# Performance work log

Hardware: AMD Instinct MI355X
Metric: run time of the kernel (lower is better)

The kernel has to match this reference:

```python
import jax, jax.numpy as jnp
import numpy as np

S, B, D, H = 2048, 32, 256, 4
EPS = 1e-5


def setup_inputs() -> dict:
    key = jax.random.key(0)
    ks = jax.random.split(key, 16)
    f32 = jnp.float32

    def w(k, shape, scale=0.05):
        return jax.random.normal(k, shape, dtype=f32) * scale

    return {
        "q": jax.random.normal(ks[0], (S, B, D), f32),
        "k": jax.random.normal(ks[1], (S, B, D), f32),
        "v": jax.random.normal(ks[2], (S, B, D), f32),
        # per-head q/k/v projections, stacked over heads [H, D, D]
        "wq": w(ks[3], (H, D, D)), "bq": jnp.zeros((H, D), f32),
        "wk": w(ks[4], (H, D, D)), "bk": jnp.zeros((H, D), f32),
        "wv": w(ks[5], (H, D, D)), "bv": jnp.zeros((H, D), f32),
        # linear_w[i] = BN -> ReLU -> Linear -> BN -> ReLU -> Linear
        "g1": jnp.ones((H, D), f32), "be1": jnp.zeros((H, D), f32),
        "wl1": w(ks[6], (H, D, D)), "bl1": jnp.zeros((H, D), f32),
        "g2": jnp.ones((H, D), f32), "be2": jnp.zeros((H, D), f32),
        "wl2": w(ks[7], (H, D, D)), "bl2": jnp.zeros((H, D), f32),
        # final MLP: [D*H -> D -> D -> D]
        "mw0": w(ks[8], (D, D * H)), "mb0": jnp.zeros((D,), f32),
        "mw1": w(ks[9], (D, D)), "mb1": jnp.zeros((D,), f32),
        "mw2": w(ks[10], (D, D)), "mb2": jnp.zeros((D,), f32),
    }


def _bn(x, gamma, beta):
    # BatchNorm1d in training mode on permuted [B, D, S] tensor == per-channel
    # normalization over (S, B) axes of the [S, B, D] tensor; biased variance.
    m = x.mean(axis=(0, 1))
    v = x.var(axis=(0, 1))
    return (x - m) * jax.lax.rsqrt(v + EPS) * gamma + beta


def _lin(x, W, b):
    return x @ W.T + b


def reference(q, k, v, wq, bq, wk, bk, wv, bv, g1, be1, wl1, bl1,
              g2, be2, wl2, bl2, mw0, mb0, mw1, mb1, mw2, mb2):
    H_ = wq.shape[0]
    xs = []
    for i in range(H_):
        # NOTE: original code reassigns q/k/v, so projections chain across heads
        q = _lin(q, wq[i], bq[i])
        k = _lin(k, wk[i], bk[i])
        v = _lin(v, wv[i], bv[i])
        w = k - q                                  # [S, B, D]
        w = jax.nn.relu(_bn(w, g1[i], be1[i]))
        w = _lin(w, wl1[i], bl1[i])
        w = jax.nn.relu(_bn(w, g2[i], be2[i]))
        w = _lin(w, wl2[i], bl2[i])
        w = jax.nn.softmax(w, axis=0)              # softmax over seq dim
        xs.append((w * v).sum(axis=0))             # [B, D]
    x = jnp.concatenate(xs, axis=-1)[None]         # [1, B, H*D]
    x = jax.nn.relu(_lin(x, mw0, mb0))
    x = jax.nn.relu(_lin(x, mw1, mb1))
    x = _lin(x, mw2, mb2)                          # [1, B, D]
    return x
```

## Files before the change

kernel.cpp:

```cpp
#include <hip/hip_runtime.h>
#include <hip/hip_bf16.h>


typedef short  s16x8 __attribute__((ext_vector_type(8)));
typedef float  f32x4 __attribute__((ext_vector_type(4)));
typedef unsigned short u16;

constexpr int NC = 16;

__device__ __forceinline__ float bu2f(u16 u) {
    union { unsigned int i; float f; } c; c.i = ((unsigned int)u) << 16; return c.f;
}
__device__ __forceinline__ float bs2f(short s) { return bu2f((u16)s); }
__device__ __forceinline__ u16 f2bu(float f) {
    union { float f; unsigned int i; } c; c.f = f;
    unsigned int u = c.i;
    u += 0x7fffu + ((u >> 16) & 1u);
    return (u16)(u >> 16);
}
__device__ __forceinline__ unsigned int pack2(float a, float b) {
    __hip_bfloat162 h = __float22bfloat162_rn(make_float2(a, b));
    union { __hip_bfloat162 h; unsigned int u; } c; c.h = h; return c.u;
}

__global__ __launch_bounds__(256) void detect_k(const unsigned int* __restrict__ qw,
                                                int* __restrict__ flag)
{
    __shared__ int cnt[256];
    const int t = threadIdx.x;
    int c = 0;
    for (int i = 0; i < 64; i++) {
        const unsigned int w = qw[t + i * 256];
        const unsigned int e = (w >> 7) & 0xFFu;
        c += (e >= 96u && e <= 141u) ? 1 : 0;
    }
    cnt[t] = c;
    __syncthreads();
    for (int s = 128; s > 0; s >>= 1) {
        if (t < s) cnt[t] += cnt[t + s];
        __syncthreads();
    }
    if (t == 0) *flag = (cnt[0] > 8192) ? 1 : 0;
}

__global__ __launch_bounds__(256) void wconv_k(
    const void* w0, const void* w1, const void* w2, const void* w3, const void* w4,
    const int* __restrict__ dflag, u16* __restrict__ dst)
{
    const void* srcs[5] = {w0, w1, w2, w3, w4};
    const int y = blockIdx.y;
    const int idx = blockIdx.x * 1024 + threadIdx.x * 4;
    u16* d = dst + y * 262144 + idx;
    if (*dflag == 0) {
        f32x4 v = *(const f32x4*)((const float*)srcs[y] + idx);
        unsigned int lo = pack2(v[0], v[1]);
        unsigned int hi = pack2(v[2], v[3]);
        *(unsigned long long*)d = ((unsigned long long)hi << 32) | lo;
    } else {
        *(unsigned long long*)d = *(const unsigned long long*)((const u16*)srcs[y] + idx);
    }
}

template<int AM, bool EXTA, int STATS>
__device__ __forceinline__ void gemm_core(
    const u16* __restrict__ A, const float* __restrict__ Af,
    const u16* __restrict__ A2, const u16* __restrict__ Qd,
    const u16* __restrict__ Wb,
    const u16* __restrict__ bias16, const float* __restrict__ biasf,
    const u16* __restrict__ g16, const float* __restrict__ gf,
    const u16* __restrict__ be16, const float* __restrict__ bef,
    const float* __restrict__ statsIn, float* __restrict__ statsOut,
    const int f32in, u16* __restrict__ C, const int bx)
{
    __shared__ __align__(16) u16 smem[8192];
    __shared__ float sc_s[256], sh_s[256];
    __shared__ float red_s[256];
    u16* As = smem;
    u16* Bs = smem + 2048;

    const int tid   = threadIdx.x;
    const int tileN = bx & 1;
    const int tileM = bx >> 1;
    const int lane  = tid & 63;
    const int wave  = tid >> 6;
    const int wm    = wave & 1;
    const int wn    = wave >> 1;
    const int lrow  = lane & 15;
    const int quad  = lane >> 4;

    if constexpr (AM != 0) {
        const int c = tid;
        float s = 0.f, q = 0.f;
#pragma unroll
        for (int i = 0; i < NC; i++) {
            s += statsIn[i * 256 + c];
            q += statsIn[(NC + i) * 256 + c];
        }
        const float mean = s * (1.f / 65536.f);
        const float var  = q * (1.f / 65536.f) - mean * mean;
        const float rstd = rsqrtf(var + 1e-5f);
        const float gg = f32in ? gf[c] : bu2f(g16[c]);
        const float bb = f32in ? bef[c] : bu2f(be16[c]);
        sc_s[c] = rstd * gg;
        sh_s[c] = bb - mean * rstd * gg;
        __syncthreads();
    }

    f32x4 acc[2][4];
#pragma unroll
    for (int i = 0; i < 2; i++)
#pragma unroll
        for (int j = 0; j < 4; j++) acc[i][j] = (f32x4){0.f, 0.f, 0.f, 0.f};

    const int  rA   = tid >> 2;
    const int  kq   = (tid & 3) << 3;
    const long rowA = (long)tileM * 64;
    const int  rowB = tileN * 128;

    for (int k0 = 0; k0 < 256; k0 += 32) {
        if (k0) __syncthreads();
        {
            const u16* gw = Wb + (rowB + rA) * 256 + k0 + kq;
            __builtin_amdgcn_global_load_lds(
                (const __attribute__((address_space(1))) void*)gw,
                (__attribute__((address_space(3))) void*)(Bs + tid * 8), 16, 0, 0);
            __builtin_amdgcn_global_load_lds(
                (const __attribute__((address_space(1))) void*)(gw + 64 * 256),
                (__attribute__((address_space(3))) void*)(Bs + 2048 + tid * 8), 16, 0, 0);
        }
        const long offA = (rowA + rA) * 256 + k0 + kq;
        if constexpr (AM == 0) {
            if (EXTA && f32in) {
                const float* p = Af + offA;
                f32x4 a = *(const f32x4*)p;
                f32x4 b = *(const f32x4*)(p + 4);
                union { s16x8 v; unsigned int w[4]; } o;
                o.w[0] = pack2(a[0], a[1]); o.w[1] = pack2(a[2], a[3]);
                o.w[2] = pack2(b[0], b[1]); o.w[3] = pack2(b[2], b[3]);
                *(s16x8*)(As + tid * 8) = o.v;
            } else {
                __builtin_amdgcn_global_load_lds(
                    (const __attribute__((address_space(1))) void*)(A + offA),
                    (__attribute__((address_space(3))) void*)(As + tid * 8), 16, 0, 0);
            }
        } else {
            s16x8 xv = *(const s16x8*)(A + offA);
            s16x8 yv;
            if constexpr (AM == 1) yv = *(const s16x8*)(A2 + offA);
            float d[8];
#pragma unroll
            for (int e = 0; e < 8; e++) {
                float x = bs2f(xv[e]);
                if constexpr (AM == 1) x -= bs2f(yv[e]);
                d[e] = fmaxf(fmaf(x, sc_s[k0 + kq + e], sh_s[k0 + kq + e]), 0.f);
            }
            union { s16x8 v; unsigned int w[4]; } o;
            o.w[0] = pack2(d[0], d[1]); o.w[1] = pack2(d[2], d[3]);
            o.w[2] = pack2(d[4], d[5]); o.w[3] = pack2(d[6], d[7]);
            *(s16x8*)(As + tid * 8) = o.v;
        }
        __syncthreads();

        s16x8 af[2], bf[4];
#pragma unroll
        for (int im = 0; im < 2; im++)
            af[im] = *(const s16x8*)(As + (wm * 32 + im * 16 + lrow) * 32 + quad * 8);
#pragma unroll
        for (int in = 0; in < 4; in++)
            bf[in] = *(const s16x8*)(Bs + (wn * 64 + in * 16 + lrow) * 32 + quad * 8);
#pragma unroll
        for (int im = 0; im < 2; im++)
#pragma unroll
            for (int in = 0; in < 4; in++)
                acc[im][in] = __builtin_amdgcn_mfma_f32_16x16x32_bf16(
                    af[im], bf[in], acc[im][in], 0, 0, 0);
    }

    __syncthreads();
    u16* Cs = smem;
#pragma unroll
    for (int in = 0; in < 4; in++) {
        const int col  = wn * 64 + in * 16 + lrow;
        const int gcol = rowB + col;
        const float bv = f32in ? biasf[gcol] : bu2f(bias16[gcol]);
#pragma unroll
        for (int im = 0; im < 2; im++) {
            const int r0 = wm * 32 + im * 16 + quad * 4;
#pragma unroll
            for (int e = 0; e < 4; e++)
                Cs[(r0 + e) * 128 + col] = f2bu(acc[im][in][e] + bv);
        }
    }
    __syncthreads();

    if constexpr (STATS != 0) {
        const int colL = tid & 127;
        const int half = tid >> 7;
        float s = 0.f, qs = 0.f;
#pragma unroll 4
        for (int r = half * 32; r < half * 32 + 32; r++) {
            float x = bu2f(Cs[r * 128 + colL]);
            if constexpr (STATS == 1) x -= bu2f(Qd[(rowA + r) * 256 + rowB + colL]);
            s += x; qs += x * x;
        }
        red_s[tid] = s;
        __syncthreads();
        float sTot = 0.f;
        if (tid < 128) sTot = red_s[tid] + red_s[tid + 128];
        __syncthreads();
        red_s[tid] = qs;
        __syncthreads();
        if (tid < 128) {
            const float qTot = red_s[tid] + red_s[tid + 128];
            const int copy = tileM & (NC - 1);
            atomicAdd(&statsOut[copy * 256 + rowB + colL], sTot);
            atomicAdd(&statsOut[(NC + copy) * 256 + rowB + colL], qTot);
        }
    }

#pragma unroll
    for (int it = 0; it < 4; it++) {
        const int r  = it * 16 + (tid >> 4);
        const int c8 = (tid & 15) * 8;
        *(s16x8*)(C + (rowA + r) * 256 + rowB + c8) = *(const s16x8*)(Cs + r * 128 + c8);
    }
}

template<int AM, bool EXTA, int STATS>
__global__ __launch_bounds__(256) void gemm_k(
    const u16* A, const float* Af, const u16* A2, const u16* Qd,
    const u16* Wb, const void* bias, const void* g, const void* be, int hoff,
    const float* statsIn, float* statsOut, const int* dflag, u16* C)
{
    const int f32in = (*dflag == 0);
    gemm_core<AM, EXTA, STATS>(A, Af, A2, Qd, Wb,
        (const u16*)bias + hoff, (const float*)bias + hoff,
        (const u16*)g + hoff,    (const float*)g + hoff,
        (const u16*)be + hoff,   (const float*)be + hoff,
        statsIn, statsOut, f32in, C, blockIdx.x);
}

template<bool EXTA>
__global__ __launch_bounds__(256) void proj2_k(
    const u16* A0, const float* A0f, const u16* W0, const void* b0, u16* C0,
    const u16* A1, const float* A1f, const u16* W1, const void* b1, u16* C1,
    int hoff, const int* dflag)
{
    const int f32in = (*dflag == 0);
    const int y = blockIdx.y;
    gemm_core<0, EXTA, 0>(
        y ? A1 : A0, y ? A1f : A0f, nullptr, nullptr, y ? W1 : W0,
        (const u16*)(y ? b1 : b0) + hoff, (const float*)(y ? b1 : b0) + hoff,
        nullptr, nullptr, nullptr, nullptr, nullptr, nullptr,
        f32in, y ? C1 : C0, blockIdx.x);
}

__global__ __launch_bounds__(256) void softmax_chunk_k(
    const u16* __restrict__ L, const u16* __restrict__ V,
    float* __restrict__ pm, float* __restrict__ pl, float* __restrict__ pa)
{
    const int d = threadIdx.x, b = blockIdx.x, ch = blockIdx.y;
    float m = -3.0e38f, l = 0.f, acc = 0.f;
    const long base = ((long)ch * 64 * 32 + b) * 256 + d;
    for (int si = 0; si < 64; si++) {
        const long idx = base + (long)si * 32 * 256;
        const float x = bu2f(L[idx]);
        const float v = bu2f(V[idx]);
        const float mn = fmaxf(m, x);
        const float c  = __expf(m - mn);
        const float e  = __expf(x - mn);
        l   = l * c + e;
        acc = acc * c + e * v;
        m = mn;
    }
    const int p = (ch * 32 + b) * 256 + d;
    pm[p] = m; pl[p] = l; pa[p] = acc;
}

__global__ __launch_bounds__(256) void softmax_merge_k(
    const float* __restrict__ pm, const float* __restrict__ pl,
    const float* __restrict__ pa, float* __restrict__ xcat, int head)
{
    const int d = threadIdx.x, b = blockIdx.x;
    float M = -3.0e38f, L = 0.f, A = 0.f;
    for (int ch = 0; ch < 32; ch++) {
        const int p = (ch * 32 + b) * 256 + d;
        const float m = pm[p], l = pl[p], a = pa[p];
        const float mn = fmaxf(M, m);
        const float c1 = __expf(M - mn), c2 = __expf(m - mn);
        L = L * c1 + l * c2;
        A = A * c1 + a * c2;
        M = mn;
    }
    xcat[b * 1024 + head * 256 + d] = A / L;
}

__global__ __launch_bounds__(256) void mlp_k(
    const float* __restrict__ xcat,
    const u16* __restrict__ mw0, const float* __restrict__ mw0f,
    const u16* __restrict__ mb0, const float* __restrict__ mb0f,
    const u16* __restrict__ mw1, const float* __restrict__ mw1f,
    const u16* __restrict__ mb1, const float* __restrict__ mb1f,
    const u16* __restrict__ mw2, const float* __restrict__ mw2f,
    const u16* __restrict__ mb2, const float* __restrict__ mb2f,
    const int* __restrict__ dflag,
    u16* __restrict__ out, float* __restrict__ outf)
{
    __shared__ float h0[1024];
    __shared__ float h1[256];
    __shared__ float h2[256];
    const int f32in = (*dflag == 0);
    const int j = threadIdx.x, b = blockIdx.x;
#pragma unroll
    for (int i = 0; i < 4; i++) h0[j + i * 256] = xcat[b * 1024 + j + i * 256];
    __syncthreads();

    float a0 = f32in ? mb0f[j] : bu2f(mb0[j]);
    if (f32in) {
        for (int k4 = 0; k4 < 256; k4++) {
            f32x4 wv = *(const f32x4*)(mw0f + j * 1024 + k4 * 4);
#pragma unroll
            for (int e = 0; e < 4; e++) a0 += h0[k4 * 4 + e] * wv[e];
        }
    } else {
        for (int k8 = 0; k8 < 128; k8++) {
            s16x8 wv = *(const s16x8*)(mw0 + j * 1024 + k8 * 8);
#pragma unroll
            for (int e = 0; e < 8; e++) a0 += h0[k8 * 8 + e] * bs2f(wv[e]);
        }
    }
    h1[j] = fmaxf(a0, 0.f);
    __syncthreads();

    float a1 = f32in ? mb1f[j] : bu2f(mb1[j]);
    if (f32in) {
        for (int k4 = 0; k4 < 64; k4++) {
            f32x4 wv = *(const f32x4*)(mw1f + j * 256 + k4 * 4);
#pragma unroll
            for (int e = 0; e < 4; e++) a1 += h1[k4 * 4 + e] * wv[e];
        }
    } else {
        for (int k8 = 0; k8 < 32; k8++) {
            s16x8 wv = *(const s16x8*)(mw1 + j * 256 + k8 * 8);
#pragma unroll
            for (int e = 0; e < 8; e++) a1 += h1[k8 * 8 + e] * bs2f(wv[e]);
        }
    }
    h2[j] = fmaxf(a1, 0.f);
    __syncthreads();

    float a2 = f32in ? mb2f[j] : bu2f(mb2[j]);
    if (f32in) {
        for (int k4 = 0; k4 < 64; k4++) {
            f32x4 wv = *(const f32x4*)(mw2f + j * 256 + k4 * 4);
#pragma unroll
            for (int e = 0; e < 4; e++) a2 += h2[k4 * 4 + e] * wv[e];
        }
    } else {
        for (int k8 = 0; k8 < 32; k8++) {
            s16x8 wv = *(const s16x8*)(mw2 + j * 256 + k8 * 8);
#pragma unroll
            for (int e = 0; e < 8; e++) a2 += h2[k8 * 8 + e] * bs2f(wv[e]);
        }
    }
    if (f32in) outf[b * 256 + j] = a2;
    else       out[b * 256 + j] = f2bu(a2);
}

extern "C" void kernel_launch(void* const* d_in, const int* in_sizes, int n_in,
                              void* d_out, int out_size, void* d_ws, size_t ws_size,
                              hipStream_t stream)
{
    const u16 *q16 = (const u16*)d_in[0], *k16 = (const u16*)d_in[1], *v16 = (const u16*)d_in[2];
    const float *qf = (const float*)d_in[0], *kf = (const float*)d_in[1], *vf = (const float*)d_in[2];

    const size_t TEN = 33554432ull;
    const size_t WBF_OFF = 2097152ull;
    const size_t BUF_OFF = 5242880ull;
    if (ws_size < BUF_OFF + 5 * TEN) return;

    char* ws = (char*)d_ws;
    int*   dflag = (int*)ws;
    float* fb    = (float*)ws;
    float* sums  = fb + 256;
    float* xcat  = sums + 8 * 2 * NC * 256;
    u16*   wbf   = (u16*)(ws + WBF_OFF);
    u16* buf[5];
    for (int i = 0; i < 5; i++) buf[i] = (u16*)(ws + BUF_OFF + (size_t)i * TEN);

    const int qsrc[4] = {-1, 0, 3, 1}, qdst[4] = {0, 3, 1, 4};
    const int ksrc[4] = {-1, 1, 4, 2}, kdst[4] = {1, 4, 2, 0};
    const int vsrc[4] = {-1, 2, 0, 3}, vdst[4] = {2, 0, 3, 1};
    const int x1i[4]  = {3, 1, 4, 2},  lgi[4]  = {4, 2, 0, 3};

    detect_k<<<dim3(1), dim3(256), 0, stream>>>((const unsigned int*)d_in[0], dflag);
    hipMemsetAsync(sums, 0, 8 * 2 * NC * 256 * sizeof(float), stream);
    wconv_k<<<dim3(256, 5), dim3(256), 0, stream>>>(
        d_in[3], d_in[5], d_in[7], d_in[11], d_in[15], dflag, wbf);

    for (int h = 0; h < 4; h++) {
        const u16* qi = h ? (const u16*)buf[qsrc[h]] : q16;
        const u16* ki = h ? (const u16*)buf[ksrc[h]] : k16;
        const u16* vi = h ? (const u16*)buf[vsrc[h]] : v16;
        u16* qo = buf[qdst[h]];
        u16* ko = buf[kdst[h]];
        u16* vo = buf[vdst[h]];
        u16* x1b = buf[x1i[h]];
        u16* lgb = buf[lgi[h]];
        const u16* Wq  = wbf + (0 * 4 + h) * 65536;
        const u16* Wk  = wbf + (1 * 4 + h) * 65536;
        const u16* Wv  = wbf + (2 * 4 + h) * 65536;
        const u16* Wl1 = wbf + (3 * 4 + h) * 65536;
        const u16* Wl2 = wbf + (4 * 4 + h) * 65536;
        float* st1 = sums + (h * 2 + 0) * 2 * NC * 256;
        float* st2 = sums + (h * 2 + 1) * 2 * NC * 256;
        float* parts = (float*)x1b;
        const int hoff = h * 256;

        if (h == 0)
            proj2_k<true><<<dim3(2048, 2), dim3(256), 0, stream>>>(
                q16, qf, Wq, d_in[4], qo, v16, vf, Wv, d_in[8], vo, hoff, dflag);
        else
            proj2_k<false><<<dim3(2048, 2), dim3(256), 0, stream>>>(
                qi, nullptr, Wq, d_in[4], qo, vi, nullptr, Wv, d_in[8], vo, hoff, dflag);

        if (h == 0)
            gemm_k<0, true, 1><<<dim3(2048), dim3(256), 0, stream>>>(
                k16, kf, nullptr, qo, Wk, d_in[6], d_in[6], d_in[6], hoff,
                nullptr, st1, dflag, ko);
        else
            gemm_k<0, false, 1><<<dim3(2048), dim3(256), 0, stream>>>(
                ki, nullptr, nullptr, qo, Wk, d_in[6], d_in[6], d_in[6], hoff,
                nullptr, st1, dflag, ko);

        gemm_k<1, false, 2><<<dim3(2048), dim3(256), 0, stream>>>(
            ko, nullptr, qo, nullptr, Wl1, d_in[12], d_in[9], d_in[10], hoff,
            st1, st2, dflag, x1b);

        gemm_k<2, false, 0><<<dim3(2048), dim3(256), 0, stream>>>(
            x1b, nullptr, nullptr, nullptr, Wl2, d_in[16], d_in[13], d_in[14], hoff,
            st2, nullptr, dflag, lgb);

        softmax_chunk_k<<<dim3(32, 32), dim3(256), 0, stream>>>(
            lgb, vo, parts, parts + 262144, parts + 524288);
        softmax_merge_k<<<dim3(32), dim3(256), 0, stream>>>(
            parts, parts + 262144, parts + 524288, xcat, h);
    }
    mlp_k<<<dim3(32), dim3(256), 0, stream>>>(
        xcat,
        (const u16*)d_in[17], (const float*)d_in[17],
        (const u16*)d_in[18], (const float*)d_in[18],
        (const u16*)d_in[19], (const float*)d_in[19],
        (const u16*)d_in[20], (const float*)d_in[20],
        (const u16*)d_in[21], (const float*)d_in[21],
        (const u16*)d_in[22], (const float*)d_in[22],
        dflag, (u16*)d_out, (float*)d_out);
}
```

Baseline: 899.1 us.

## Double-buffer GEMM K-loop tiles in LDS and remap block-to-tile order

Splits the K-loop into stage/compute lambdas with two LDS buffers, so the next 32-wide K slice is loaded while MFMAs run on the current one. This removes one barrier per iteration and overlaps global-load latency with compute. It also remaps the block index so consecutive blocks are spread across tile rows, likely for XCD/cache locality. LDS use grows to 24KB, which may reduce occupancy.

```diff
diff --git a/kernel.cpp b/kernel.cpp
--- a/kernel.cpp
+++ b/kernel.cpp
@@ -72,15 +72,14 @@
     const float* __restrict__ statsIn, float* __restrict__ statsOut,
     const int f32in, u16* __restrict__ C, const int bx)
 {
-    __shared__ __align__(16) u16 smem[8192];
+    __shared__ __align__(16) u16 smem[12288];
     __shared__ float sc_s[256], sh_s[256];
     __shared__ float red_s[256];
-    u16* As = smem;
-    u16* Bs = smem + 2048;
 
     const int tid   = threadIdx.x;
-    const int tileN = bx & 1;
-    const int tileM = bx >> 1;
+    const int work  = ((bx & 7) << 8) | (bx >> 3);
+    const int tileN = work & 1;
+    const int tileM = work >> 1;
     const int lane  = tid & 63;
     const int wave  = tid >> 6;
     const int wm    = wave & 1;
@@ -117,26 +116,25 @@
     const long rowA = (long)tileM * 64;
     const int  rowB = tileN * 128;
 
-    for (int k0 = 0; k0 < 256; k0 += 32) {
-        if (k0) __syncthreads();
-        {
-            const u16* gw = Wb + (rowB + rA) * 256 + k0 + kq;
-            __builtin_amdgcn_global_load_lds(
-                (const __attribute__((address_space(1))) void*)gw,
-                (__attribute__((address_space(3))) void*)(Bs + tid * 8), 16, 0, 0);
-            __builtin_amdgcn_global_load_lds(
-                (const __attribute__((address_space(1))) void*)(gw + 64 * 256),
-                (__attribute__((address_space(3))) void*)(Bs + 2048 + tid * 8), 16, 0, 0);
-        }
+    auto stage = [&](int k0, int b) {
+        u16* As = smem + b * 6144;
+        u16* Bs = As + 2048;
+        const u16* gw = Wb + (rowB + rA) * 256 + k0 + kq;
+        __builtin_amdgcn_global_load_lds(
+            (const __attribute__((address_space(1))) void*)gw,
+            (__attribute__((address_space(3))) void*)(Bs + tid * 8), 16, 0, 0);
+        __builtin_amdgcn_global_load_lds(
+            (const __attribute__((address_space(1))) void*)(gw + 64 * 256),
+            (__attribute__((address_space(3))) void*)(Bs + 2048 + tid * 8), 16, 0, 0);
         const long offA = (rowA + rA) * 256 + k0 + kq;
         if constexpr (AM == 0) {
             if (EXTA && f32in) {
                 const float* p = Af + offA;
                 f32x4 a = *(const f32x4*)p;
-                f32x4 b = *(const f32x4*)(p + 4);
+                f32x4 bb = *(const f32x4*)(p + 4);
                 union { s16x8 v; unsigned int w[4]; } o;
                 o.w[0] = pack2(a[0], a[1]); o.w[1] = pack2(a[2], a[3]);
-                o.w[2] = pack2(b[0], b[1]); o.w[3] = pack2(b[2], b[3]);
+                o.w[2] = pack2(bb[0], bb[1]); o.w[3] = pack2(bb[2], bb[3]);
                 *(s16x8*)(As + tid * 8) = o.v;
             } else {
                 __builtin_amdgcn_global_load_lds(
@@ -159,8 +157,11 @@
             o.w[2] = pack2(d[4], d[5]); o.w[3] = pack2(d[6], d[7]);
             *(s16x8*)(As + tid * 8) = o.v;
         }
-        __syncthreads();
-
+    };
+
+    auto comp = [&](int b) {
+        const u16* As = smem + b * 6144;
+        const u16* Bs = As + 2048;
         s16x8 af[2], bf[4];
 #pragma unroll
         for (int im = 0; im < 2; im++)
@@ -174,7 +175,19 @@
             for (int in = 0; in < 4; in++)
                 acc[im][in] = __builtin_amdgcn_mfma_f32_16x16x32_bf16(
                     af[im], bf[in], acc[im][in], 0, 0, 0);
-    }
+    };
+
+    stage(0, 0);
+    __syncthreads();
+    int cur = 0;
+#pragma unroll
+    for (int t = 0; t < 7; ++t) {
+        stage((t + 1) * 32, cur ^ 1);
+        comp(cur);
+        __syncthreads();
+        cur ^= 1;
+    }
+    comp(cur);
 
     __syncthreads();
     u16* Cs = smem;
```

Result: faster. 856.9 us (-4.7%).

## Stage full weight tile in swizzled LDS and keep A fragments in registers

Applied to the files above, without the earlier changes.

Drops the 8-step K loop, which had a barrier per step. The whole 128x256 bf16 weight tile is now loaded into LDS once, using an XOR swizzle to avoid bank conflicts. The A operand (including the fused BN/ReLU transform) is read straight from global memory into registers as MFMA fragments, so A no longer goes through LDS. Block indices are also remapped so consecutive blocks spread across XCDs. The cost is 64KB of LDS and many more VGPRs, which lowers occupancy.

```diff
diff --git a/kernel.cpp b/kernel.cpp
--- a/kernel.cpp
+++ b/kernel.cpp
@@ -72,21 +72,23 @@
     const float* __restrict__ statsIn, float* __restrict__ statsOut,
     const int f32in, u16* __restrict__ C, const int bx)
 {
-    __shared__ __align__(16) u16 smem[8192];
+    __shared__ __align__(16) u16 smem[32768];
     __shared__ float sc_s[256], sh_s[256];
     __shared__ float red_s[256];
-    u16* As = smem;
-    u16* Bs = smem + 2048;
 
     const int tid   = threadIdx.x;
-    const int tileN = bx & 1;
-    const int tileM = bx >> 1;
+    const int work  = ((bx & 7) << 8) | (bx >> 3);
+    const int tileN = work & 1;
+    const int tileM = work >> 1;
     const int lane  = tid & 63;
     const int wave  = tid >> 6;
     const int wm    = wave & 1;
     const int wn    = wave >> 1;
     const int lrow  = lane & 15;
     const int quad  = lane >> 4;
+
+    const long rowA = (long)tileM * 64;
+    const int  rowB = tileN * 128;
 
     if constexpr (AM != 0) {
         const int c = tid;
@@ -106,74 +108,105 @@
         __syncthreads();
     }
 
+    {
+        char* lds = (char*)smem;
+#pragma unroll
+        for (int i = 0; i < 16; i++) {
+            const int L    = i * 4096 + tid * 16;
+            const int row  = L >> 9;
+            const int colB = L & 511;
+            const int scol = colB ^ ((row & 7) << 4);
+            const u16* src = Wb + (size_t)(rowB + row) * 256 + (scol >> 1);
+            __builtin_amdgcn_global_load_lds(
+                (const __attribute__((address_space(1))) void*)src,
+                (__attribute__((address_space(3))) void*)(lds + L), 16, 0, 0);
+        }
+    }
+
+    s16x8 areg[8][2];
+    const int arow0 = wm * 32 + lrow;
+    if constexpr (AM == 0) {
+        if (EXTA && f32in) {
+#pragma unroll
+            for (int t = 0; t < 8; t++)
+#pragma unroll
+                for (int im = 0; im < 2; im++) {
+                    const float* p = Af + (rowA + arow0 + im * 16) * 256 + t * 32 + quad * 8;
+                    f32x4 a = *(const f32x4*)p;
+                    f32x4 b = *(const f32x4*)(p + 4);
+                    union { s16x8 v; unsigned int w[4]; } o;
+                    o.w[0] = pack2(a[0], a[1]); o.w[1] = pack2(a[2], a[3]);
+                    o.w[2] = pack2(b[0], b[1]); o.w[3] = pack2(b[2], b[3]);
+                    areg[t][im] = o.v;
+                }
+        } else {
+#pragma unroll
+            for (int t = 0; t < 8; t++)
+#pragma unroll
+                for (int im = 0; im < 2; im++)
+                    areg[t][im] = *(const s16x8*)(A + (rowA + arow0 + im * 16) * 256 + t * 32 + quad * 8);
+        }
+    } else {
+        s16x8 xv[8][2];
+        s16x8 yv[8][2];
+#pragma unroll
+        for (int t = 0; t < 8; t++)
+#pragma unroll
+            for (int im = 0; im < 2; im++) {
+                const long off = (rowA + arow0 + im * 16) * 256 + t * 32 + quad * 8;
+                xv[t][im] = *(const s16x8*)(A + off);
+                if constexpr (AM == 1) yv[t][im] = *(const s16x8*)(A2 + off);
+            }
+#pragma unroll
+        for (int t = 0; t < 8; t++) {
+            const int kb = t * 32 + quad * 8;
+            const f32x4 sc0 = *(const f32x4*)(sc_s + kb);
+            const f32x4 sc1 = *(const f32x4*)(sc_s + kb + 4);
+            const f32x4 sh0 = *(const f32x4*)(sh_s + kb);
+            const f32x4 sh1 = *(const f32x4*)(sh_s + kb + 4);
+#pragma unroll
+            for (int im = 0; im < 2; im++) {
+                float d[8];
+#pragma unroll
+                for (int e = 0; e < 8; e++) {
+                    float x = bs2f(xv[t][im][e]);
+                    if constexpr (AM == 1) x -= bs2f(yv[t][im][e]);
+                    const float sc = (e < 4) ? sc0[e] : sc1[e - 4];
+                    const float sh = (e < 4) ? sh0[e] : sh1[e - 4];
+                    d[e] = fmaxf(fmaf(x, sc, sh), 0.f);
+                }
+                union { s16x8 v; unsigned int w[4]; } o;
+                o.w[0] = pack2(d[0], d[1]); o.w[1] = pack2(d[2], d[3]);
+                o.w[2] = pack2(d[4], d[5]); o.w[3] = pack2(d[6], d[7]);
+                areg[t][im] = o.v;
+            }
+        }
+    }
+
+    __syncthreads();
+
     f32x4 acc[2][4];
 #pragma unroll
     for (int i = 0; i < 2; i++)
 #pragma unroll
         for (int j = 0; j < 4; j++) acc[i][j] = (f32x4){0.f, 0.f, 0.f, 0.f};
 
-    const int  rA   = tid >> 2;
-    const int  kq   = (tid & 3) << 3;
-    const long rowA = (long)tileM * 64;
-    const int  rowB = tileN * 128;
-
-    for (int k0 = 0; k0 < 256; k0 += 32) {
-        if (k0) __syncthreads();
-        {
-            const u16* gw = Wb + (rowB + rA) * 256 + k0 + kq;
-            __builtin_amdgcn_global_load_lds(
-                (const __attribute__((address_space(1))) void*)gw,
-                (__attribute__((address_space(3))) void*)(Bs + tid * 8), 16, 0, 0);
-            __builtin_amdgcn_global_load_lds(
-                (const __attribute__((address_space(1))) void*)(gw + 64 * 256),
-                (__attribute__((address_space(3))) void*)(Bs + 2048 + tid * 8), 16, 0, 0);
-        }
-        const long offA = (rowA + rA) * 256 + k0 + kq;
-        if constexpr (AM == 0) {
-            if (EXTA && f32in) {
-                const float* p = Af + offA;
-                f32x4 a = *(const f32x4*)p;
-                f32x4 b = *(const f32x4*)(p + 4);
-                union { s16x8 v; unsigned int w[4]; } o;
-                o.w[0] = pack2(a[0], a[1]); o.w[1] = pack2(a[2], a[3]);
-                o.w[2] = pack2(b[0], b[1]); o.w[3] = pack2(b[2], b[3]);
-                *(s16x8*)(As + tid * 8) = o.v;
-            } else {
-                __builtin_amdgcn_global_load_lds(
-                    (const __attribute__((address_space(1))) void*)(A + offA),
-                    (__attribute__((address_space(3))) void*)(As + tid * 8), 16, 0, 0);
-            }
-        } else {
-            s16x8 xv = *(const s16x8*)(A + offA);
-            s16x8 yv;
-            if constexpr (AM == 1) yv = *(const s16x8*)(A2 + offA);
-            float d[8];
-#pragma unroll
-            for (int e = 0; e < 8; e++) {
-                float x = bs2f(xv[e]);
-                if constexpr (AM == 1) x -= bs2f(yv[e]);
-                d[e] = fmaxf(fmaf(x, sc_s[k0 + kq + e], sh_s[k0 + kq + e]), 0.f);
-            }
-            union { s16x8 v; unsigned int w[4]; } o;
-            o.w[0] = pack2(d[0], d[1]); o.w[1] = pack2(d[2], d[3]);
-            o.w[2] = pack2(d[4], d[5]); o.w[3] = pack2(d[6], d[7]);
-            *(s16x8*)(As + tid * 8) = o.v;
-        }
-        __syncthreads();
-
-        s16x8 af[2], bf[4];
-#pragma unroll
-        for (int im = 0; im < 2; im++)
-            af[im] = *(const s16x8*)(As + (wm * 32 + im * 16 + lrow) * 32 + quad * 8);
-#pragma unroll
-        for (int in = 0; in < 4; in++)
-            bf[in] = *(const s16x8*)(Bs + (wn * 64 + in * 16 + lrow) * 32 + quad * 8);
+    const char* BsC = (const char*)smem;
+#pragma unroll
+    for (int t = 0; t < 8; t++) {
+        s16x8 bf[4];
+#pragma unroll
+        for (int in = 0; in < 4; in++) {
+            const int brow = wn * 64 + in * 16 + lrow;
+            const int bcol = (t * 64 + quad * 16) ^ ((lrow & 7) << 4);
+            bf[in] = *(const s16x8*)(BsC + brow * 512 + bcol);
+        }
 #pragma unroll
         for (int im = 0; im < 2; im++)
 #pragma unroll
             for (int in = 0; in < 4; in++)
                 acc[im][in] = __builtin_amdgcn_mfma_f32_16x16x32_bf16(
-                    af[im], bf[in], acc[im][in], 0, 0, 0);
+                    areg[t][im], bf[in], acc[im][in], 0, 0, 0);
     }
 
     __syncthreads();
```

Measured after the change: 1.127 ms. 1.25x slower.

## Pre-swizzle weights into MFMA fragment layout and double K-step per stage

Applied to the files above, without the earlier changes.

The weight conversion kernel now writes bf16 weights in a fragment-major layout that matches the MFMA lane order, so the GEMM's LDS reads become contiguous per-lane 16-byte loads. The GEMM K loop now processes 64 columns per stage (two MFMA k-steps) with a larger LDS buffer, which halves the number of barriers. Block indices are remapped so that consecutive blocks spread across tiles, which may improve cache or XCD locality. The A tile is also staged in the fragment layout. The cost is more LDS per block, which can reduce occupancy, and more complex address arithmetic.

```diff
diff --git a/kernel.cpp b/kernel.cpp
--- a/kernel.cpp
+++ b/kernel.cpp
@@ -48,16 +48,28 @@
     const int* __restrict__ dflag, u16* __restrict__ dst)
 {
     const void* srcs[5] = {w0, w1, w2, w3, w4};
-    const int y = blockIdx.y;
-    const int idx = blockIdx.x * 1024 + threadIdx.x * 4;
-    u16* d = dst + y * 262144 + idx;
+    const int y    = blockIdx.y;
+    const int head = blockIdx.x >> 5;
+    const int cb   = blockIdx.x & 31;
+    const int c    = cb * 256 + threadIdx.x;
+    const int l    = c & 63;
+    const int ntl  = (c >> 6) & 7;
+    const int half = (c >> 9) & 1;
+    const int kk   = c >> 10;
+    const int n    = half * 128 + ntl * 16 + (l & 15);
+    const int k    = kk * 32 + ((l >> 4) & 3) * 8;
+    const size_t so = (size_t)head * 65536 + (size_t)n * 256 + k;
+    u16* d = dst + (size_t)y * 262144 + (size_t)head * 65536 + (size_t)c * 8;
     if (*dflag == 0) {
-        f32x4 v = *(const f32x4*)((const float*)srcs[y] + idx);
-        unsigned int lo = pack2(v[0], v[1]);
-        unsigned int hi = pack2(v[2], v[3]);
-        *(unsigned long long*)d = ((unsigned long long)hi << 32) | lo;
+        const float* sf = (const float*)srcs[y] + so;
+        f32x4 a = *(const f32x4*)sf;
+        f32x4 b = *(const f32x4*)(sf + 4);
+        union { s16x8 v; unsigned int w[4]; } o;
+        o.w[0] = pack2(a[0], a[1]); o.w[1] = pack2(a[2], a[3]);
+        o.w[2] = pack2(b[0], b[1]); o.w[3] = pack2(b[2], b[3]);
+        *(s16x8*)d = o.v;
     } else {
-        *(unsigned long long*)d = *(const unsigned long long*)((const u16*)srcs[y] + idx);
+        *(s16x8*)d = *(const s16x8*)((const u16*)srcs[y] + so);
     }
 }
 
@@ -72,21 +84,25 @@
     const float* __restrict__ statsIn, float* __restrict__ statsOut,
     const int f32in, u16* __restrict__ C, const int bx)
 {
-    __shared__ __align__(16) u16 smem[8192];
+    __shared__ __align__(16) u16 smem[12288];
     __shared__ float sc_s[256], sh_s[256];
     __shared__ float red_s[256];
     u16* As = smem;
-    u16* Bs = smem + 2048;
+    u16* Bs = smem + 4096;
 
     const int tid   = threadIdx.x;
-    const int tileN = bx & 1;
-    const int tileM = bx >> 1;
+    const int work  = ((bx & 7) << 8) | (bx >> 3);
+    const int tileN = work & 1;
+    const int tileM = work >> 1;
     const int lane  = tid & 63;
     const int wave  = tid >> 6;
     const int wm    = wave & 1;
     const int wn    = wave >> 1;
     const int lrow  = lane & 15;
     const int quad  = lane >> 4;
+
+    const long rowA = (long)tileM * 64;
+    const int  rowB = tileN * 128;
 
     if constexpr (AM != 0) {
         const int c = tid;
@@ -112,68 +128,82 @@
 #pragma unroll
         for (int j = 0; j < 4; j++) acc[i][j] = (f32x4){0.f, 0.f, 0.f, 0.f};
 
-    const int  rA   = tid >> 2;
-    const int  kq   = (tid & 3) << 3;
-    const long rowA = (long)tileM * 64;
-    const int  rowB = tileN * 128;
-
-    for (int k0 = 0; k0 < 256; k0 += 32) {
-        if (k0) __syncthreads();
-        {
-            const u16* gw = Wb + (rowB + rA) * 256 + k0 + kq;
+    for (int s = 0; s < 4; s++) {
+        if (s) __syncthreads();
+
+#pragma unroll
+        for (int j = 0; j < 4; j++) {
+            const int cp = j * 256 + tid;
+            const u16* src = Wb
+                + (size_t)((2 * s + (cp >> 9)) * 2 + tileN) * 4096
+                + (size_t)(cp & 511) * 8;
             __builtin_amdgcn_global_load_lds(
-                (const __attribute__((address_space(1))) void*)gw,
-                (__attribute__((address_space(3))) void*)(Bs + tid * 8), 16, 0, 0);
-            __builtin_amdgcn_global_load_lds(
-                (const __attribute__((address_space(1))) void*)(gw + 64 * 256),
-                (__attribute__((address_space(3))) void*)(Bs + 2048 + tid * 8), 16, 0, 0);
-        }
-        const long offA = (rowA + rA) * 256 + k0 + kq;
-        if constexpr (AM == 0) {
-            if (EXTA && f32in) {
-                const float* p = Af + offA;
-                f32x4 a = *(const f32x4*)p;
-                f32x4 b = *(const f32x4*)(p + 4);
+                (const __attribute__((address_space(1))) void*)src,
+                (__attribute__((address_space(3))) void*)(Bs + cp * 8), 16, 0, 0);
+        }
+
+#pragma unroll
+        for (int j = 0; j < 2; j++) {
+            const int cp  = j * 256 + tid;
+            const int kk  = cp >> 8;
+            const int wmi = (cp >> 7) & 1;
+            const int imi = (cp >> 6) & 1;
+            const int l   = cp & 63;
+            const long row = rowA + wmi * 32 + imi * 16 + (l & 15);
+            const int  col = s * 64 + kk * 32 + ((l >> 4) & 3) * 8;
+            const long off = row * 256 + col;
+            if constexpr (AM == 0) {
+                if (EXTA && f32in) {
+                    const float* p = Af + off;
+                    f32x4 a = *(const f32x4*)p;
+                    f32x4 b = *(const f32x4*)(p + 4);
+                    union { s16x8 v; unsigned int w[4]; } o;
+                    o.w[0] = pack2(a[0], a[1]); o.w[1] = pack2(a[2], a[3]);
+                    o.w[2] = pack2(b[0], b[1]); o.w[3] = pack2(b[2], b[3]);
+                    *(s16x8*)(As + cp * 8) = o.v;
+                } else {
+                    __builtin_amdgcn_global_load_lds(
+                        (const __attribute__((address_space(1))) void*)(A + off),
+                        (__attribute__((address_space(3))) void*)(As + cp * 8), 16, 0, 0);
+                }
+            } else {
+                s16x8 xv = *(const s16x8*)(A + off);
+                s16x8 yv;
+                if constexpr (AM == 1) yv = *(const s16x8*)(A2 + off);
+                float d[8];
+#pragma unroll
+                for (int e = 0; e < 8; e++) {
+                    float x = bs2f(xv[e]);
+                    if constexpr (AM == 1) x -= bs2f(yv[e]);
+                    d[e] = fmaxf(fmaf(x, sc_s[col + e], sh_s[col + e]), 0.f);
+                }
                 union { s16x8 v; unsigned int w[4]; } o;
-                o.w[0] = pack2(a[0], a[1]); o.w[1] = pack2(a[2], a[3]);
-                o.w[2] = pack2(b[0], b[1]); o.w[3] = pack2(b[2], b[3]);
-                *(s16x8*)(As + tid * 8) = o.v;
-            } else {
-                __builtin_amdgcn_global_load_lds(
-                    (const __attribute__((address_space(1))) void*)(A + offA),
-                    (__attribute__((address_space(3))) void*)(As + tid * 8), 16, 0, 0);
+                o.w[0] = pack2(d[0], d[1]); o.w[1] = pack2(d[2], d[3]);
+                o.w[2] = pack2(d[4], d[5]); o.w[3] = pack2(d[6], d[7]);
+                *(s16x8*)(As + cp * 8) = o.v;
             }
-        } else {
-            s16x8 xv = *(const s16x8*)(A + offA);
-            s16x8 yv;
-            if constexpr (AM == 1) yv = *(const s16x8*)(A2 + offA);
-            float d[8];
-#pragma unroll
-            for (int e = 0; e < 8; e++) {
-                float x = bs2f(xv[e]);
-                if constexpr (AM == 1) x -= bs2f(yv[e]);
-                d[e] = fmaxf(fmaf(x, sc_s[k0 + kq + e], sh_s[k0 + kq + e]), 0.f);
-            }
-            union { s16x8 v; unsigned int w[4]; } o;
-            o.w[0] = pack2(d[0], d[1]); o.w[1] = pack2(d[2], d[3]);
-            o.w[2] = pack2(d[4], d[5]); o.w[3] = pack2(d[6], d[7]);
-            *(s16x8*)(As + tid * 8) = o.v;
-        }
-        __syncthreads();
-
-        s16x8 af[2], bf[4];
-#pragma unroll
-        for (int im = 0; im < 2; im++)
-            af[im] = *(const s16x8*)(As + (wm * 32 + im * 16 + lrow) * 32 + quad * 8);
-#pragma unroll
-        for (int in = 0; in < 4; in++)
-            bf[in] = *(const s16x8*)(Bs + (wn * 64 + in * 16 + lrow) * 32 + quad * 8);
-#pragma unroll
-        for (int im = 0; im < 2; im++)
+        }
+
+        __syncthreads();
+
+        s16x8 af[2][2], bf[2][4];
+#pragma unroll
+        for (int kk = 0; kk < 2; kk++) {
+#pragma unroll
+            for (int im = 0; im < 2; im++)
+                af[kk][im] = *(const s16x8*)(As + (((kk * 2 + wm) * 2 + im) * 64 + lane) * 8);
 #pragma unroll
             for (int in = 0; in < 4; in++)
-                acc[im][in] = __builtin_amdgcn_mfma_f32_16x16x32_bf16(
-                    af[im], bf[in], acc[im][in], 0, 0, 0);
+                bf[kk][in] = *(const s16x8*)(Bs + ((kk * 8 + wn * 4 + in) * 64 + lane) * 8);
+        }
+#pragma unroll
+        for (int kk = 0; kk < 2; kk++)
+#pragma unroll
+            for (int im = 0; im < 2; im++)
+#pragma unroll
+                for (int in = 0; in < 4; in++)
+                    acc[im][in] = __builtin_amdgcn_mfma_f32_16x16x32_bf16(
+                        af[kk][im], bf[kk][in], acc[im][in], 0, 0, 0);
     }
 
     __syncthreads();
@@ -395,7 +425,7 @@
 
     detect_k<<<dim3(1), dim3(256), 0, stream>>>((const unsigned int*)d_in[0], dflag);
     hipMemsetAsync(sums, 0, 8 * 2 * NC * 256 * sizeof(float), stream);
-    wconv_k<<<dim3(256, 5), dim3(256), 0, stream>>>(
+    wconv_k<<<dim3(128, 5), dim3(256), 0, stream>>>(
         d_in[3], d_in[5], d_in[7], d_in[11], d_in[15], dflag, wbf);
 
     for (int h = 0; h < 4; h++) {
```

After: 858.2 us. 4.5% less time.
